# Optimization experiments

Measured on AMD Instinct MI355X. Metric: run time of the kernel, lower is better.

The kernel has to match this reference:

```python
import jax, jax.numpy as jnp
import numpy as np

N_NODES = 50000
N_EDGES = 800000
HIDDEN = 128
N_GRAPHS = 256
N_CLASSES = 10


def setup_inputs() -> dict:
    key = jax.random.key(0)
    ks = jax.random.split(key, 9)
    x = jax.random.normal(ks[0], (N_NODES, HIDDEN), dtype=jnp.float32)
    edge_index = jax.random.randint(ks[1], (2, N_EDGES), 0, N_NODES, dtype=jnp.int64)
    batch = jnp.sort(jax.random.randint(ks[2], (N_NODES,), 0, N_GRAPHS, dtype=jnp.int64))
    s = 1.0 / np.sqrt(HIDDEN)
    W1 = jax.random.uniform(ks[3], (HIDDEN, HIDDEN), jnp.float32, -s, s)
    b1 = jax.random.uniform(ks[4], (HIDDEN,), jnp.float32, -s, s)
    W2 = jax.random.uniform(ks[5], (HIDDEN, HIDDEN), jnp.float32, -s, s)
    b2 = jax.random.uniform(ks[6], (HIDDEN,), jnp.float32, -s, s)
    Wl = jax.random.uniform(ks[7], (HIDDEN, N_CLASSES), jnp.float32, -s, s)
    bl = jax.random.uniform(ks[8], (N_CLASSES,), jnp.float32, -s, s)
    return {"x": x, "edge_index": edge_index, "batch": batch,
            "W1": W1, "b1": b1, "W2": W2, "b2": b2, "Wl": Wl, "bl": bl}


def _gin_conv(x, src, dst, W1, b1, W2, b2):
    # GINConv, eps=0: nn(x + sum_{j->i} x_j); messages flow src -> dst
    agg = jax.ops.segment_sum(x[src], dst, num_segments=N_NODES)
    h = x + agg
    h = jnp.maximum(h @ W1 + b1, 0.0) @ W2 + b2  # shared 2-layer MLP
    return h


def reference(x, edge_index, batch, W1, b1, W2, b2, Wl, bl):
    src, dst = edge_index[0], edge_index[1]
    h = jnp.maximum(_gin_conv(x, src, dst, W1, b1, W2, b2), 0.0)
    h = jnp.maximum(_gin_conv(h, src, dst, W1, b1, W2, b2), 0.0)
    h = _gin_conv(h, src, dst, W1, b1, W2, b2)
    # global mean pool over graphs
    sums = jax.ops.segment_sum(h, batch, num_segments=N_GRAPHS)
    cnt = jax.ops.segment_sum(jnp.ones((N_NODES,), h.dtype), batch, num_segments=N_GRAPHS)
    pooled = sums / jnp.maximum(cnt, 1.0)[:, None]
    # dropout is identity in eval mode
    return pooled @ Wl + bl
```

## Files before the change

kernel.cpp:

```cpp
#include <hip/hip_runtime.h>

#define N_NODES  50000
#define N_EDGES  800000
#define HIDDEN   128
#define N_GRAPHS 256
#define N_CLASSES 10
#define WLD 136
#define E_HALF 400000
#define POISON 0xAAAAAAAAu

typedef short short8 __attribute__((ext_vector_type(8)));
typedef float floatx4 __attribute__((ext_vector_type(4)));

__device__ inline unsigned short bf16_rtne(float x) {
    unsigned u = __float_as_uint(x);
    unsigned r = ((u >> 16) & 1u) + 0x7fffu;
    return (unsigned short)((u + r) >> 16);
}

__global__ void prep_kernel(const int* __restrict__ dst, int* __restrict__ deg0, int* __restrict__ deg1,
                            int* __restrict__ epos,
                            const float* __restrict__ W1, unsigned short* __restrict__ W1b,
                            const float* __restrict__ W2, unsigned short* __restrict__ W2b,
                            const float4* __restrict__ X, uint4* __restrict__ Xb,
                            int* __restrict__ counter) {
    int b = blockIdx.x;
    if (b < 3125) {
        int e = b * 256 + threadIdx.x;
        int* degp = (e < E_HALF) ? deg0 : deg1;
        int old = atomicAdd(&degp[dst[e]], 1);
        epos[e] = (int)((unsigned)old - POISON);
    } else if (b < 3253) {
        int idx = (b - 3125) * 256 + threadIdx.x;
        if (idx == 0) counter[0] = 0;
        int which = idx >> 14, sub = idx & (HIDDEN * HIDDEN - 1);
        int k = sub >> 7, n = sub & 127;
        (which ? W2b : W1b)[n * HIDDEN + k] = bf16_rtne((which ? W2 : W1)[sub]);
    } else {
        int i = (b - 3253) * 256 + threadIdx.x;
        int n = i >> 4, c = i & 15;
        float4 a = X[(size_t)n * 32 + c * 2], v = X[(size_t)n * 32 + c * 2 + 1];
        uint4 o;
        o.x = (unsigned)bf16_rtne(a.x) | ((unsigned)bf16_rtne(a.y) << 16);
        o.y = (unsigned)bf16_rtne(a.z) | ((unsigned)bf16_rtne(a.w) << 16);
        o.z = (unsigned)bf16_rtne(v.x) | ((unsigned)bf16_rtne(v.y) << 16);
        o.w = (unsigned)bf16_rtne(v.z) | ((unsigned)bf16_rtne(v.w) << 16);
        Xb[(size_t)(c >> 2) * N_NODES * 4 + (size_t)n * 4 + (c & 3)] = o;
    }
}

__global__ void offsets_kernel(int* __restrict__ deg0, int* __restrict__ deg1,
                               int* __restrict__ row_start, int* __restrict__ counter) {
    int n = blockIdx.x * blockDim.x + threadIdx.x;
    int d0 = 0, dT = 0;
    if (n < N_NODES) {
        d0 = (int)((unsigned)deg0[n] - POISON);
        int d1 = (int)((unsigned)deg1[n] - POISON);
        dT = d0 + d1;
    }
    int lane = threadIdx.x & 63;
    int incl = dT;
    #pragma unroll
    for (int o = 1; o < 64; o <<= 1) {
        int v = __shfl_up(incl, o, 64);
        if (lane >= o) incl += v;
    }
    int excl = incl - dT;
    int total = __shfl(incl, 63, 64);
    int base = 0;
    if (lane == 0) base = atomicAdd(counter, total);
    base = __shfl(base, 0, 64);
    if (n < N_NODES) {
        row_start[n] = base + excl;
        deg0[n] = d0;
        deg1[n] = dT;
    }
}

__global__ void place_kernel(const int* __restrict__ src, const int* __restrict__ dst,
                             const int* __restrict__ epos, const int* __restrict__ row_start,
                             const int* __restrict__ deg0, int* __restrict__ csr_src) {
    int e = blockIdx.x * blockDim.x + threadIdx.x;
    if (e >= N_EDGES) return;
    int d = dst[e];
    int pos = row_start[d] + epos[e];
    if (e >= E_HALF) pos += deg0[d];
    csr_src[pos] = src[e];
}

__device__ inline void acc_bf2(unsigned d, float& f0, float& f1) {
    f0 += __uint_as_float(d << 16);
    f1 += __uint_as_float(d & 0xffff0000u);
}
__device__ inline void acc8(const uint4 v, float* a) {
    acc_bf2(v.x, a[0], a[1]); acc_bf2(v.y, a[2], a[3]);
    acc_bf2(v.z, a[4], a[5]); acc_bf2(v.w, a[6], a[7]);
}

__global__ void agg_kernel(const uint4* __restrict__ Xb, const int* __restrict__ row_start,
                           const int* __restrict__ deg, const int* __restrict__ csr_src,
                           uint4* __restrict__ Tb ) {
    int s = blockIdx.x & 3;
    int n = (blockIdx.x >> 2) * 64 + (threadIdx.x >> 2);
    int chunk = threadIdx.x & 3;
    if (n >= N_NODES) return;
    const uint4* Ts = Xb + (size_t)s * (N_NODES * 4);
    float a[8];
    #pragma unroll
    for (int j = 0; j < 8; ++j) a[j] = 0.f;
    {
        uint4 v = Ts[(size_t)n * 4 + chunk];
        acc8(v, a);
    }
    int rs = row_start[n], d = deg[n];
    int i = 0;
    for (; i + 4 <= d; i += 4) {
        int s0 = csr_src[rs + i + 0];
        int s1 = csr_src[rs + i + 1];
        int s2 = csr_src[rs + i + 2];
        int s3 = csr_src[rs + i + 3];
        uint4 v0 = Ts[(size_t)s0 * 4 + chunk];
        uint4 v1 = Ts[(size_t)s1 * 4 + chunk];
        uint4 v2 = Ts[(size_t)s2 * 4 + chunk];
        uint4 v3 = Ts[(size_t)s3 * 4 + chunk];
        acc8(v0, a); acc8(v1, a); acc8(v2, a); acc8(v3, a);
    }
    for (; i < d; ++i) {
        int s0 = csr_src[rs + i];
        uint4 v0 = Ts[(size_t)s0 * 4 + chunk];
        acc8(v0, a);
    }
    uint4 o;
    o.x = (unsigned)bf16_rtne(a[0]) | ((unsigned)bf16_rtne(a[1]) << 16);
    o.y = (unsigned)bf16_rtne(a[2]) | ((unsigned)bf16_rtne(a[3]) << 16);
    o.z = (unsigned)bf16_rtne(a[4]) | ((unsigned)bf16_rtne(a[5]) << 16);
    o.w = (unsigned)bf16_rtne(a[6]) | ((unsigned)bf16_rtne(a[7]) << 16);
    Tb[(size_t)n * 16 + s * 4 + chunk] = o;
}

__global__ __launch_bounds__(256)
void mm_mfma(const unsigned short* __restrict__ Ab,
             const unsigned short* __restrict__ Bw,
             const float* __restrict__ bias,
             unsigned short* __restrict__ Cb, int relu, int blocked) {
    __shared__ unsigned short WhS[64 * WLD];

    int t = threadIdx.x;
    int col_base = blockIdx.y * 64;
    {
        const short8* gh = (const short8*)(Bw + (size_t)col_base * HIDDEN);
        #pragma unroll
        for (int i = 0; i < 4; ++i) {
            int idx = i * 256 + t;
            int row = idx >> 4, kk = (idx & 15) * 8;
            *(short8*)(WhS + row * WLD + kk) = gh[idx];
        }
    }
    __syncthreads();

    int w = t >> 6;
    int l = t & 63;
    int lane16 = l & 15;
    int quad = l >> 4;
    int row_base = blockIdx.x * 128 + w * 32;

    floatx4 acc[2][4];
    #pragma unroll
    for (int m = 0; m < 2; ++m)
        #pragma unroll
        for (int nt = 0; nt < 4; ++nt) acc[m][nt] = (floatx4){0.f, 0.f, 0.f, 0.f};

    #pragma unroll
    for (int kc = 0; kc < 4; ++kc) {
        int k0 = kc * 32 + quad * 8;
        short8 af[2];
        #pragma unroll
        for (int m = 0; m < 2; ++m) {
            int r = row_base + m * 16 + lane16;
            if (r < N_NODES) af[m] = *(const short8*)(Ab + (size_t)r * HIDDEN + k0);
            else             af[m] = (short8){0,0,0,0,0,0,0,0};
        }
        short8 bh[4];
        #pragma unroll
        for (int nt = 0; nt < 4; ++nt)
            bh[nt] = *(const short8*)(WhS + (nt * 16 + lane16) * WLD + k0);
        #pragma unroll
        for (int m = 0; m < 2; ++m)
            #pragma unroll
            for (int nt = 0; nt < 4; ++nt)
                acc[m][nt] = __builtin_amdgcn_mfma_f32_16x16x32_bf16(af[m], bh[nt], acc[m][nt], 0, 0, 0);
    }
    #pragma unroll
    for (int nt = 0; nt < 4; ++nt) {
        int col = col_base + nt * 16 + lane16;
        float b = bias[col];
        #pragma unroll
        for (int m = 0; m < 2; ++m) {
            #pragma unroll
            for (int reg = 0; reg < 4; ++reg) {
                int r = row_base + m * 16 + quad * 4 + reg;
                if (r < N_NODES) {
                    float o = acc[m][nt][reg] + b;
                    if (relu) o = fmaxf(o, 0.f);
                    size_t oi = blocked
                        ? ((size_t)(col >> 5) * N_NODES + r) * 32 + (col & 31)
                        : (size_t)r * HIDDEN + col;
                    Cb[oi] = bf16_rtne(o);
                }
            }
        }
    }
}

__global__ void pool_head_kernel(const unsigned short* __restrict__ H, const int* __restrict__ batch,
                                 const float* __restrict__ Wl, const float* __restrict__ bl,
                                 float* __restrict__ out) {
    int g = blockIdx.x;
    int t = threadIdx.x;
    __shared__ int bounds[2];
    __shared__ float acc2[2 * HIDDEN];
    __shared__ float mean[HIDDEN];

    if (t < 2) {
        int target = g + t;
        int lo = 0, hi = N_NODES;
        while (lo < hi) {
            int mid = (lo + hi) >> 1;
            if (batch[mid] < target) lo = mid + 1; else hi = mid;
        }
        bounds[t] = lo;
    }
    __syncthreads();
    int r0 = bounds[0], r1 = bounds[1];

    int c = t & 127, half = t >> 7;
    float s = 0.f;
    for (int r = r0 + half; r < r1; r += 2)
        s += __uint_as_float((unsigned)H[(size_t)r * HIDDEN + c] << 16);
    acc2[half * HIDDEN + c] = s;
    __syncthreads();
    if (t < HIDDEN) {
        float cntf = (float)(r1 - r0);
        mean[t] = (acc2[t] + acc2[HIDDEN + t]) / fmaxf(cntf, 1.0f);
    }
    __syncthreads();
    if (t < N_CLASSES) {
        float o = bl[t];
        #pragma unroll 8
        for (int k = 0; k < HIDDEN; ++k) o = fmaf(mean[k], Wl[k * N_CLASSES + t], o);
        out[(size_t)g * N_CLASSES + t] = o;
    }
}

extern "C" void kernel_launch(void* const* d_in, const int* in_sizes, int n_in,
                              void* d_out, int out_size, void* d_ws, size_t ws_size,
                              hipStream_t stream) {
    const float* x   = (const float*)d_in[0];
    const int*   ei  = (const int*)d_in[1];
    const int*   bat = (const int*)d_in[2];
    const float* W1  = (const float*)d_in[3];
    const float* b1  = (const float*)d_in[4];
    const float* W2  = (const float*)d_in[5];
    const float* b2  = (const float*)d_in[6];
    const float* Wl  = (const float*)d_in[7];
    const float* bl  = (const float*)d_in[8];
    float* out = (float*)d_out;

    const int* src = ei;
    const int* dst = ei + N_EDGES;

    char* w = (char*)d_ws;
    size_t off = 0;
    auto alloc = [&](size_t bytes) { void* p = w + off; off = (off + bytes + 255) & ~(size_t)255; return p; };
    unsigned short* g_bf  = (unsigned short*)alloc((size_t)N_NODES * HIDDEN * 2);
    unsigned short* t_bf  = (unsigned short*)alloc((size_t)N_NODES * HIDDEN * 2);
    unsigned short* z_bf  = (unsigned short*)alloc((size_t)N_NODES * HIDDEN * 2);
    int*   deg0    = (int*)  alloc((size_t)N_NODES * 4);
    int*   deg1    = (int*)  alloc((size_t)N_NODES * 4);
    int*   rowst   = (int*)  alloc((size_t)N_NODES * 4);
    int*   epos    = (int*)  alloc((size_t)N_EDGES * 4);
    int*   csr_src = (int*)  alloc((size_t)N_EDGES * 4);
    int*   counter = (int*)  alloc(256);
    unsigned short* w1b = (unsigned short*)alloc((size_t)HIDDEN * HIDDEN * 2);
    unsigned short* w2b = (unsigned short*)alloc((size_t)HIDDEN * HIDDEN * 2);
    (void)ws_size; (void)in_sizes; (void)n_in; (void)out_size;


    prep_kernel<<<6378, 256, 0, stream>>>(dst, deg0, deg1, epos, W1, w1b, W2, w2b,
                                          (const float4*)x, (uint4*)g_bf, counter);
    offsets_kernel<<<(N_NODES + 255) / 256, 256, 0, stream>>>(deg0, deg1, rowst, counter);
    place_kernel<<<(N_EDGES + 255) / 256, 256, 0, stream>>>(src, dst, epos, rowst, deg0, csr_src);

    const int agg_grid = 4 * ((N_NODES + 63) / 64);
    const dim3 mm_grid((N_NODES + 127) / 128, 2);

    agg_kernel<<<agg_grid, 256, 0, stream>>>((const uint4*)g_bf, rowst, deg1, csr_src, (uint4*)t_bf);
    mm_mfma<<<mm_grid, 256, 0, stream>>>(t_bf, w1b, b1, z_bf, 1, 0);
    mm_mfma<<<mm_grid, 256, 0, stream>>>(z_bf, w2b, b2, g_bf, 1, 1);
    agg_kernel<<<agg_grid, 256, 0, stream>>>((const uint4*)g_bf, rowst, deg1, csr_src, (uint4*)t_bf);
    mm_mfma<<<mm_grid, 256, 0, stream>>>(t_bf, w1b, b1, z_bf, 1, 0);
    mm_mfma<<<mm_grid, 256, 0, stream>>>(z_bf, w2b, b2, g_bf, 1, 1);
    agg_kernel<<<agg_grid, 256, 0, stream>>>((const uint4*)g_bf, rowst, deg1, csr_src, (uint4*)t_bf);
    mm_mfma<<<mm_grid, 256, 0, stream>>>(t_bf, w1b, b1, z_bf, 1, 0);
    mm_mfma<<<mm_grid, 256, 0, stream>>>(z_bf, w2b, b2, t_bf, 0, 0);

    pool_head_kernel<<<N_GRAPHS, 256, 0, stream>>>(t_bf, bat, Wl, bl, out);
}
```

Baseline: 344.2 us.

## Fuse the two MLP GEMMs into one kernel with the hidden activation kept in LDS

Replaces the pair of mm_mfma launches per GIN layer with a single mlp2_kernel. The first GEMM is computed transposed (W1 rows as the A operand, node rows as the B operand), and its bias+ReLU output is stored in shared memory in a padded per-node layout. The second GEMM then reads it from LDS together with the full W2 staged in LDS. This removes the global write and re-read of the intermediate z buffer and one launch per layer. In exchange each block uses about 70KB of LDS and the grid is halved, which reduces occupancy and parallelism. The last layer also runs in place on t_bf despite the __restrict__ qualifiers.

```diff
diff --git a/kernel.cpp b/kernel.cpp
--- a/kernel.cpp
+++ b/kernel.cpp
@@ -6,6 +6,7 @@
 #define N_GRAPHS 256
 #define N_CLASSES 10
 #define WLD 136
+#define ZLD 136
 #define E_HALF 400000
 #define POISON 0xAAAAAAAAu
 
@@ -139,69 +140,113 @@
 }
 
 __global__ __launch_bounds__(256)
-void mm_mfma(const unsigned short* __restrict__ Ab,
-             const unsigned short* __restrict__ Bw,
-             const float* __restrict__ bias,
-             unsigned short* __restrict__ Cb, int relu, int blocked) {
-    __shared__ unsigned short WhS[64 * WLD];
+void mlp2_kernel(const unsigned short* __restrict__ Ab,
+                 const unsigned short* __restrict__ W1b,
+                 const float* __restrict__ b1,
+                 const unsigned short* __restrict__ W2b,
+                 const float* __restrict__ b2,
+                 unsigned short* __restrict__ Cb, int relu2, int blocked) {
+    __shared__ unsigned short W2S[HIDDEN * WLD];
+    __shared__ unsigned short zS[128 * ZLD];
 
     int t = threadIdx.x;
-    int col_base = blockIdx.y * 64;
     {
-        const short8* gh = (const short8*)(Bw + (size_t)col_base * HIDDEN);
-        #pragma unroll
-        for (int i = 0; i < 4; ++i) {
+        const short8* gh = (const short8*)W2b;
+        #pragma unroll
+        for (int i = 0; i < 8; ++i) {
             int idx = i * 256 + t;
             int row = idx >> 4, kk = (idx & 15) * 8;
-            *(short8*)(WhS + row * WLD + kk) = gh[idx];
-        }
-    }
-    __syncthreads();
-
-    int w = t >> 6;
-    int l = t & 63;
-    int lane16 = l & 15;
-    int quad = l >> 4;
-    int row_base = blockIdx.x * 128 + w * 32;
-
-    floatx4 acc[2][4];
+            *(short8*)(W2S + row * WLD + kk) = gh[idx];
+        }
+    }
+    __syncthreads();
+
+    int w = t >> 6, l = t & 63;
+    int lane16 = l & 15, quad = l >> 4;
+    int node_base = blockIdx.x * 128;
+
+    floatx4 acc[2][8];
     #pragma unroll
     for (int m = 0; m < 2; ++m)
         #pragma unroll
-        for (int nt = 0; nt < 4; ++nt) acc[m][nt] = (floatx4){0.f, 0.f, 0.f, 0.f};
+        for (int nt = 0; nt < 8; ++nt) acc[m][nt] = (floatx4){0.f, 0.f, 0.f, 0.f};
 
     #pragma unroll
     for (int kc = 0; kc < 4; ++kc) {
         int k0 = kc * 32 + quad * 8;
-        short8 af[2];
+        short8 bt[8];
+        #pragma unroll
+        for (int nt = 0; nt < 8; ++nt) {
+            int r = node_base + nt * 16 + lane16;
+            if (r < N_NODES) bt[nt] = *(const short8*)(Ab + (size_t)r * HIDDEN + k0);
+            else             bt[nt] = (short8){0,0,0,0,0,0,0,0};
+        }
+        short8 aw[2];
         #pragma unroll
         for (int m = 0; m < 2; ++m) {
-            int r = row_base + m * 16 + lane16;
-            if (r < N_NODES) af[m] = *(const short8*)(Ab + (size_t)r * HIDDEN + k0);
-            else             af[m] = (short8){0,0,0,0,0,0,0,0};
-        }
-        short8 bh[4];
-        #pragma unroll
-        for (int nt = 0; nt < 4; ++nt)
-            bh[nt] = *(const short8*)(WhS + (nt * 16 + lane16) * WLD + k0);
+            int zc = (2 * w + m) * 16 + lane16;
+            aw[m] = *(const short8*)(W1b + (size_t)zc * HIDDEN + k0);
+        }
         #pragma unroll
         for (int m = 0; m < 2; ++m)
             #pragma unroll
-            for (int nt = 0; nt < 4; ++nt)
-                acc[m][nt] = __builtin_amdgcn_mfma_f32_16x16x32_bf16(af[m], bh[nt], acc[m][nt], 0, 0, 0);
-    }
-    #pragma unroll
-    for (int nt = 0; nt < 4; ++nt) {
-        int col = col_base + nt * 16 + lane16;
-        float b = bias[col];
+            for (int nt = 0; nt < 8; ++nt)
+                acc[m][nt] = __builtin_amdgcn_mfma_f32_16x16x32_bf16(aw[m], bt[nt], acc[m][nt], 0, 0, 0);
+    }
+    #pragma unroll
+    for (int m = 0; m < 2; ++m) {
+        int zc0 = (2 * w + m) * 16 + quad * 4;
+        float4 bb = *(const float4*)(b1 + zc0);
+        #pragma unroll
+        for (int nt = 0; nt < 8; ++nt) {
+            int node = nt * 16 + lane16;
+            ushort4 pk;
+            pk.x = bf16_rtne(fmaxf(acc[m][nt][0] + bb.x, 0.f));
+            pk.y = bf16_rtne(fmaxf(acc[m][nt][1] + bb.y, 0.f));
+            pk.z = bf16_rtne(fmaxf(acc[m][nt][2] + bb.z, 0.f));
+            pk.w = bf16_rtne(fmaxf(acc[m][nt][3] + bb.w, 0.f));
+            *(ushort4*)(zS + node * ZLD + zc0) = pk;
+        }
+    }
+    __syncthreads();
+
+    floatx4 acc2[2][8];
+    #pragma unroll
+    for (int m = 0; m < 2; ++m)
+        #pragma unroll
+        for (int nt = 0; nt < 8; ++nt) acc2[m][nt] = (floatx4){0.f, 0.f, 0.f, 0.f};
+
+    #pragma unroll
+    for (int kc = 0; kc < 4; ++kc) {
+        int k0 = kc * 32 + quad * 8;
+        short8 az[2];
+        #pragma unroll
+        for (int m = 0; m < 2; ++m) {
+            int lr = w * 32 + m * 16 + lane16;
+            az[m] = *(const short8*)(zS + lr * ZLD + k0);
+        }
+        short8 bh[8];
+        #pragma unroll
+        for (int nt = 0; nt < 8; ++nt)
+            bh[nt] = *(const short8*)(W2S + (nt * 16 + lane16) * WLD + k0);
+        #pragma unroll
+        for (int m = 0; m < 2; ++m)
+            #pragma unroll
+            for (int nt = 0; nt < 8; ++nt)
+                acc2[m][nt] = __builtin_amdgcn_mfma_f32_16x16x32_bf16(az[m], bh[nt], acc2[m][nt], 0, 0, 0);
+    }
+    #pragma unroll
+    for (int nt = 0; nt < 8; ++nt) {
+        int col = nt * 16 + lane16;
+        float b = b2[col];
         #pragma unroll
         for (int m = 0; m < 2; ++m) {
             #pragma unroll
             for (int reg = 0; reg < 4; ++reg) {
-                int r = row_base + m * 16 + quad * 4 + reg;
+                int r = node_base + w * 32 + m * 16 + quad * 4 + reg;
                 if (r < N_NODES) {
-                    float o = acc[m][nt][reg] + b;
-                    if (relu) o = fmaxf(o, 0.f);
+                    float o = acc2[m][nt][reg] + b;
+                    if (relu2) o = fmaxf(o, 0.f);
                     size_t oi = blocked
                         ? ((size_t)(col >> 5) * N_NODES + r) * 32 + (col & 31)
                         : (size_t)r * HIDDEN + col;
@@ -274,7 +319,6 @@
     auto alloc = [&](size_t bytes) { void* p = w + off; off = (off + bytes + 255) & ~(size_t)255; return p; };
     unsigned short* g_bf  = (unsigned short*)alloc((size_t)N_NODES * HIDDEN * 2);
     unsigned short* t_bf  = (unsigned short*)alloc((size_t)N_NODES * HIDDEN * 2);
-    unsigned short* z_bf  = (unsigned short*)alloc((size_t)N_NODES * HIDDEN * 2);
     int*   deg0    = (int*)  alloc((size_t)N_NODES * 4);
     int*   deg1    = (int*)  alloc((size_t)N_NODES * 4);
     int*   rowst   = (int*)  alloc((size_t)N_NODES * 4);
@@ -285,24 +329,20 @@
     unsigned short* w2b = (unsigned short*)alloc((size_t)HIDDEN * HIDDEN * 2);
     (void)ws_size; (void)in_sizes; (void)n_in; (void)out_size;
 
-
     prep_kernel<<<6378, 256, 0, stream>>>(dst, deg0, deg1, epos, W1, w1b, W2, w2b,
                                           (const float4*)x, (uint4*)g_bf, counter);
     offsets_kernel<<<(N_NODES + 255) / 256, 256, 0, stream>>>(deg0, deg1, rowst, counter);
     place_kernel<<<(N_EDGES + 255) / 256, 256, 0, stream>>>(src, dst, epos, rowst, deg0, csr_src);
 
     const int agg_grid = 4 * ((N_NODES + 63) / 64);
-    const dim3 mm_grid((N_NODES + 127) / 128, 2);
+    const int mlp_grid = (N_NODES + 127) / 128;
 
     agg_kernel<<<agg_grid, 256, 0, stream>>>((const uint4*)g_bf, rowst, deg1, csr_src, (uint4*)t_bf);
-    mm_mfma<<<mm_grid, 256, 0, stream>>>(t_bf, w1b, b1, z_bf, 1, 0);
-    mm_mfma<<<mm_grid, 256, 0, stream>>>(z_bf, w2b, b2, g_bf, 1, 1);
+    mlp2_kernel<<<mlp_grid, 256, 0, stream>>>(t_bf, w1b, b1, w2b, b2, g_bf, 1, 1);
     agg_kernel<<<agg_grid, 256, 0, stream>>>((const uint4*)g_bf, rowst, deg1, csr_src, (uint4*)t_bf);
-    mm_mfma<<<mm_grid, 256, 0, stream>>>(t_bf, w1b, b1, z_bf, 1, 0);
-    mm_mfma<<<mm_grid, 256, 0, stream>>>(z_bf, w2b, b2, g_bf, 1, 1);
+    mlp2_kernel<<<mlp_grid, 256, 0, stream>>>(t_bf, w1b, b1, w2b, b2, g_bf, 1, 1);
     agg_kernel<<<agg_grid, 256, 0, stream>>>((const uint4*)g_bf, rowst, deg1, csr_src, (uint4*)t_bf);
-    mm_mfma<<<mm_grid, 256, 0, stream>>>(t_bf, w1b, b1, z_bf, 1, 0);
-    mm_mfma<<<mm_grid, 256, 0, stream>>>(z_bf, w2b, b2, t_bf, 0, 0);
+    mlp2_kernel<<<mlp_grid, 256, 0, stream>>>(t_bf, w1b, b1, w2b, b2, t_bf, 0, 0);
 
     pool_head_kernel<<<N_GRAPHS, 256, 0, stream>>>(t_bf, bat, Wl, bl, out);
 }
```

Result: no change. 343.7 us (-0.1%).
